# Kernel optimization log

Measured on AMD Instinct MI355X. Metric: run time of the kernel, lower is better.

The kernel has to match this reference:

```python
import jax, jax.numpy as jnp
import numpy as np

NUM_HEADS = 16


def setup_inputs() -> dict:
    key = jax.random.key(0)
    ks = jax.random.split(key, 7)
    dim, hd = 1024, 64
    B, H, W = 64, 14, 14  # B = batch * num_windows, 14x14 window
    x = jax.random.normal(ks[0], (B, H, W, dim), dtype=jnp.float32)
    qkv_w = jax.random.normal(ks[1], (dim, 3 * dim), dtype=jnp.float32) * (dim ** -0.5)
    qkv_b = jnp.zeros((3 * dim,), dtype=jnp.float32)
    proj_w = jax.random.normal(ks[2], (dim, dim), dtype=jnp.float32) * (dim ** -0.5)
    proj_b = jnp.zeros((dim,), dtype=jnp.float32)
    rel_pos_h = jax.random.normal(ks[3], (2 * H - 1, hd), dtype=jnp.float32) * 0.02
    rel_pos_w = jax.random.normal(ks[4], (2 * W - 1, hd), dtype=jnp.float32) * 0.02
    return {"x": x, "qkv_w": qkv_w, "qkv_b": qkv_b, "proj_w": proj_w,
            "proj_b": proj_b, "rel_pos_h": rel_pos_h, "rel_pos_w": rel_pos_w}


def reference(x, qkv_w, qkv_b, proj_w, proj_b, rel_pos_h, rel_pos_w):
    B, H, W, dim = x.shape
    nH = NUM_HEADS
    hd = dim // nH
    scale = hd ** -0.5

    # qkv projection: [B, HW, 3*dim]
    qkv = x.reshape(B, H * W, dim) @ qkv_w + qkv_b
    # -> [3, nH, B, HW, hd] -> [3, nH*B, HW, hd]
    qkv = qkv.reshape(B, H * W, 3, nH, hd).transpose(2, 3, 0, 1, 4)
    qkv = qkv.reshape(3, nH * B, H * W, hd)
    q, k, v = qkv[0], qkv[1], qkv[2]

    # scaled QK^T: [nH*B, HW, HW]
    attn = jnp.einsum('bqc,bkc->bqk', q * scale, k)

    # decomposed relative position bias (q_size == k_size, no interpolation)
    Rh = rel_pos_h[jnp.arange(H)[:, None] - jnp.arange(H)[None, :] + (H - 1)]  # [H,H,hd]
    Rw = rel_pos_w[jnp.arange(W)[:, None] - jnp.arange(W)[None, :] + (W - 1)]  # [W,W,hd]
    r_q = q.reshape(nH * B, H, W, hd)
    rel_h = jnp.einsum('bhwc,hkc->bhwk', r_q, Rh)  # [nH*B,H,W,H]
    rel_w = jnp.einsum('bhwc,wkc->bhwk', r_q, Rw)  # [nH*B,H,W,W]
    attn = (attn.reshape(nH * B, H, W, H, W)
            + rel_h[:, :, :, :, None]
            + rel_w[:, :, :, None, :]).reshape(nH * B, H * W, H * W)

    attn = jax.nn.softmax(attn, axis=-1)
    out = attn @ v  # [nH*B, HW, hd]

    # merge heads: [nH,B,H,W,hd] -> [B,H,W,dim]
    out = out.reshape(nH, B, H, W, hd).transpose(1, 2, 3, 0, 4).reshape(B, H, W, dim)
    return out @ proj_w + proj_b
```

## Files before the change

### kernel.cpp

```cpp
#include <hip/hip_runtime.h>
#include <cstdint>
#include <cstddef>

typedef unsigned short u16;
typedef unsigned int u32;
typedef float f32x4 __attribute__((ext_vector_type(4)));
typedef float f32x2 __attribute__((ext_vector_type(2)));
typedef short short8 __attribute__((ext_vector_type(8)));

#define HW 196
#define DIM 1024
#define HD 64
#define SP 208
#define SPV 224
#define NBH 1024

__device__ __forceinline__ float bf2f(u16 x){
  union { u32 u; float f; } c; c.u = ((u32)x) << 16; return c.f;
}
__device__ __forceinline__ u16 f2bf(float f){
  union { float f; u32 u; } c; c.f = f;
  return (u16)((c.u + 0x7fffu + ((c.u >> 16) & 1u)) >> 16);
}
__device__ __forceinline__ u32 cvtpk_bf16(float lo, float hi){
  u32 r;
  asm("v_cvt_pk_bf16_f32 %0, %1, %2" : "=v"(r) : "v"(lo), "v"(hi));
  return r;
}
#define LGKM_FENCE() do { \
    asm volatile("s_waitcnt lgkmcnt(0)" ::: "memory"); \
    __builtin_amdgcn_sched_barrier(0); \
  } while (0)
#define WAITV4() asm volatile("s_waitcnt vmcnt(4)" ::: "memory")
#define BAR() __builtin_amdgcn_s_barrier()

typedef __attribute__((address_space(3))) void lds_void_t;
typedef __attribute__((address_space(1))) const void glb_void_t;
__device__ __forceinline__ void gload_lds16(const void* g, void* l){
  __builtin_amdgcn_global_load_lds((glb_void_t*)g, (lds_void_t*)l, 16, 0, 0);
}

__global__ __launch_bounds__(256) void k_xcvt(const float* __restrict__ x,
                                              u16* __restrict__ xb, int n8){
  int i = blockIdx.x * 256 + threadIdx.x;
  if (i < n8){
    const f32x4* p = (const f32x4*)(x + (size_t)i * 8);
    f32x4 v0 = p[0], v1 = p[1];
    short8 t;
    #pragma unroll
    for (int e = 0; e < 4; ++e){
      t[e]   = (short)f2bf(v0[e]);
      t[4+e] = (short)f2bf(v1[e]);
    }
    *(short8*)(xb + (size_t)i * 8) = t;
  }
}

__global__ __launch_bounds__(256) void k_rprep(const float* __restrict__ rph,
                                               const float* __restrict__ rpw,
                                               u16* __restrict__ rphb,
                                               u16* __restrict__ rpwb){
  int r = threadIdx.x >> 3, cc = (threadIdx.x & 7) * 8;
  #pragma unroll
  for (int t = 0; t < 2; ++t){
    const float* src = t ? rpw : rph;
    u16* dst = t ? rpwb : rphb;
    short8 v;
    #pragma unroll
    for (int e = 0; e < 8; ++e)
      v[e] = (r < 27) ? (short)f2bf(src[(size_t)r * 64 + cc + e]) : (short)0;
    *(short8*)(dst + (size_t)r * 64 + cc) = v;
  }
}

__global__ __launch_bounds__(256) void k_wT(const float* __restrict__ w,
                                            u16* __restrict__ wT, int K, int N){
  __shared__ float t[32][33];
  int n0 = blockIdx.x * 32, k0 = blockIdx.y * 32;
  int c = threadIdx.x & 31, rr = threadIdx.x >> 5;
  #pragma unroll
  for (int i = 0; i < 4; ++i){
    int r = rr + i*8;
    t[r][c] = w[(size_t)(k0 + r) * N + n0 + c];
  }
  __syncthreads();
  #pragma unroll
  for (int i = 0; i < 4; ++i){
    int r = rr + i*8;
    wT[(size_t)(n0 + r) * K + k0 + c] = f2bf(t[c][r]);
  }
}

template<int MODE, bool SW>
__global__ __launch_bounds__(512, 2) void k_g256(const u16* __restrict__ Ab,
    const u16* __restrict__ Bt, const float* __restrict__ bias,
    u16* __restrict__ qg, u16* __restrict__ kg, u16* __restrict__ vTg,
    float* __restrict__ outf, int K, int N, int ntm, int ntn, int cyoff)
{
  extern __shared__ __align__(16) u16 smem[];
  const int tid = threadIdx.x;
  const int lane = tid & 63, wv = tid >> 6;
  const int wr = wv >> 2, wc = wv & 3;
  const int l16 = lane & 15, lk = lane >> 4;

  const int nwg = ntm * ntn;
  int bid = blockIdx.x;
  int q8 = nwg >> 3, r8 = nwg & 7;
  int xcd = bid & 7, loc = bid >> 3;
  int wgid = (xcd < r8 ? xcd*(q8+1) : r8*(q8+1) + (xcd - r8)*q8) + loc;
  int gsz = 8 * ntn;
  int g = wgid / gsz, rem = wgid - g * gsz;
  int gm = ntm - g * 8; if (gm > 8) gm = 8;
  int ry = g * 8 + rem % gm;
  int cy = rem / gm;
  const size_t m0 = (size_t)ry * 256;
  const size_t n0 = (size_t)(cyoff + cy) * 256;
  const int nk = K >> 6;

  auto off = [&](int d, int ab, int ks){ return ((d*2 + ab)*2 + ks) * 8192; };

  auto stageH = [&](int d, int ab, int ks, int tile){
    const u16* src = ab ? Bt : Ab;
    size_t rb = ab ? n0 : m0;
    int c = (lane & 3) ^ ((lane >> 3) & 3);
    #pragma unroll
    for (int i = 0; i < 2; ++i){
      int rh = 32*wv + 16*i + (lane >> 2);
      gload_lds16(src + (rb + rh) * (size_t)K + tile*64 + ks*32 + c*8,
                  smem + off(d, ab, ks) + (32*wv + 16*i) * 32);
    }
  };
  auto ldA = [&](short8* a, int d, int ks, int h){
    #pragma unroll
    for (int m2 = 0; m2 < 4; ++m2){
      int r = wr*128 + h*64 + m2*16 + l16;
      a[m2] = *(const short8*)(smem + off(d,0,ks) + r*32 + ((lk ^ ((r>>1)&3)) << 3));
    }
  };
  auto ldB = [&](short8* b, int d, int ks){
    #pragma unroll
    for (int ni = 0; ni < 4; ++ni){
      int r = wc*64 + ni*16 + l16;
      b[ni] = *(const short8*)(smem + off(d,1,ks) + r*32 + ((lk ^ ((r>>1)&3)) << 3));
    }
  };

  f32x4 acc[8][4] = {};
  auto mm = [&](int h, short8* a, short8* b){
    __builtin_amdgcn_s_setprio(1);
    #pragma unroll
    for (int m2 = 0; m2 < 4; ++m2)
      #pragma unroll
      for (int ni = 0; ni < 4; ++ni){
        if constexpr (SW)
          acc[h*4+m2][ni] = __builtin_amdgcn_mfma_f32_16x16x32_bf16(b[ni], a[m2], acc[h*4+m2][ni], 0, 0, 0);
        else
          acc[h*4+m2][ni] = __builtin_amdgcn_mfma_f32_16x16x32_bf16(a[m2], b[ni], acc[h*4+m2][ni], 0, 0, 0);
      }
    __builtin_amdgcn_s_setprio(0);
  };

  stageH(0, 0, 0, 0); stageH(0, 1, 0, 0); stageH(0, 0, 1, 0); stageH(0, 1, 1, 0);
  WAITV4(); BAR();

  #pragma unroll 1
  for (int kt = 0; kt < nk; ++kt){
    const int d = kt & 1, dn = d ^ 1;
    const int tn = (kt + 1 < nk) ? kt + 1 : nk - 1;
    short8 a[4], b0[4], b1[4];
    ldA(a, d, 0, 0); ldB(b0, d, 0);
    stageH(dn, 0, 0, tn);
    BAR(); LGKM_FENCE();
    mm(0, a, b0);
    BAR();
    ldA(a, d, 0, 1);
    stageH(dn, 1, 0, tn);
    WAITV4();
    BAR(); LGKM_FENCE();
    mm(1, a, b0);
    BAR();
    ldA(a, d, 1, 0); ldB(b1, d, 1);
    stageH(dn, 0, 1, tn);
    BAR(); LGKM_FENCE();
    mm(0, a, b1);
    BAR();
    ldA(a, d, 1, 1);
    stageH(dn, 1, 1, tn);
    WAITV4();
    BAR(); LGKM_FENCE();
    mm(1, a, b1);
    BAR();
  }

  const int rowb = (int)m0 + wr*128;
  const int colb = (int)n0 + wc*64;
  if constexpr (MODE == 1){
    #pragma unroll
    for (int mi = 0; mi < 8; ++mi){
      int r = rowb + mi*16 + l16;
      float* orow = outf + (size_t)r * N;
      #pragma unroll
      for (int ni = 0; ni < 4; ++ni){
        int c0 = colb + ni*16 + lk*4;
        f32x4 bz = *(const f32x4*)(bias + c0);
        f32x4 v = acc[mi][ni] + bz;
        *(f32x4*)(orow + c0) = v;
      }
    }
  } else if constexpr (SW){
    const int t3 = colb >> 10;
    u16* dst0 = (t3 == 0) ? qg : kg;
    #pragma unroll
    for (int mi = 0; mi < 8; ++mi){
      int r = rowb + mi*16 + l16;
      int b = r / 196, n = r - b * 196;
      #pragma unroll
      for (int ni = 0; ni < 4; ++ni){
        int rr2 = ((colb & 1023) + ni*16);
        int hh = rr2 >> 6, ccb = (rr2 & 63) + lk*4;
        const float* bz = bias + colb + ni*16 + lk*4;
        u32 w0 = cvtpk_bf16(acc[mi][ni][0] + bz[0], acc[mi][ni][1] + bz[1]);
        u32 w1 = cvtpk_bf16(acc[mi][ni][2] + bz[2], acc[mi][ni][3] + bz[3]);
        u32* dst = (u32*)(dst0 + ((size_t)(hh*64 + b) * SP + n) * HD + ccb);
        dst[0] = w0; dst[1] = w1;
      }
    }
  } else {
    #pragma unroll
    for (int mi = 0; mi < 8; ++mi){
      int r4 = rowb + mi*16 + lk*4;
      int b = r4 / 196, n4 = r4 - b * 196;
      #pragma unroll
      for (int ni = 0; ni < 4; ++ni){
        int rr2 = ((colb & 1023) + ni*16);
        int hh = rr2 >> 6, cc = (rr2 & 63) + l16;
        float bz = bias[colb + ni*16 + l16];
        u32 w0 = cvtpk_bf16(acc[mi][ni][0] + bz, acc[mi][ni][1] + bz);
        u32 w1 = cvtpk_bf16(acc[mi][ni][2] + bz, acc[mi][ni][3] + bz);
        u32* dst = (u32*)(vTg + ((size_t)(hh*64 + b) * HD + cc) * SPV + n4);
        dst[0] = w0; dst[1] = w1;
      }
    }
  }
}

__global__ __launch_bounds__(256) void k_attn(
    const u16* __restrict__ qg, const u16* __restrict__ kg, const u16* __restrict__ vTg,
    const u16* __restrict__ rphb, const u16* __restrict__ rpwb,
    u16* __restrict__ ao)
{
  __shared__ __align__(16) char smem[4 * 7168];
  const int tid = threadIdx.x, lane = tid & 63, wvi = tid >> 6;
  const int l16 = lane & 15, lk = lane >> 4;
  char*  wbase = smem + wvi * 7168;
  float* relT  = (float*)wbase;
  float* relg  = (float*)(wbase + 4160);
  char*  pbase = wbase;

  int b = blockIdx.x;
  int sb = (b & 7) * 416 + (b >> 3);
  int j  = sb * 4 + wvi;
  int bh = j / 13;
  int mt = j - bh * 13;
  const int hh = bh >> 6, bb = bh & 63;
  const u16* qb = qg  + (size_t)bh * SP * HD;
  const u16* kb = kg  + (size_t)bh * SP * HD;
  const u16* vb = vTg + (size_t)bh * HD * SPV;

  const short8 a0 = *(const short8*)(qb + (size_t)(mt*16 + l16) * HD + lk*8);
  const short8 a1 = *(const short8*)(qb + (size_t)(mt*16 + l16) * HD + 32 + lk*8);

  {
    f32x4 z = {0.f,0.f,0.f,0.f};
    f32x4 racc[2][2] = {{z,z},{z,z}};
    #pragma unroll
    for (int dt = 0; dt < 2; ++dt){
      short8 h0 = *(const short8*)(rphb + (size_t)(dt*16 + l16) * 64 + lk*8);
      short8 h1 = *(const short8*)(rphb + (size_t)(dt*16 + l16) * 64 + 32 + lk*8);
      short8 w0 = *(const short8*)(rpwb + (size_t)(dt*16 + l16) * 64 + lk*8);
      short8 w1 = *(const short8*)(rpwb + (size_t)(dt*16 + l16) * 64 + 32 + lk*8);
      racc[0][dt] = __builtin_amdgcn_mfma_f32_16x16x32_bf16(h0, a0, racc[0][dt], 0, 0, 0);
      racc[0][dt] = __builtin_amdgcn_mfma_f32_16x16x32_bf16(h1, a1, racc[0][dt], 0, 0, 0);
      racc[1][dt] = __builtin_amdgcn_mfma_f32_16x16x32_bf16(w0, a0, racc[1][dt], 0, 0, 0);
      racc[1][dt] = __builtin_amdgcn_mfma_f32_16x16x32_bf16(w1, a1, racc[1][dt], 0, 0, 0);
    }
    #pragma unroll
    for (int t = 0; t < 2; ++t)
      #pragma unroll
      for (int dt = 0; dt < 2; ++dt)
        #pragma unroll
        for (int i = 0; i < 4; ++i)
          relT[l16*65 + t*32 + dt*16 + lk*4 + i] = racc[t][dt][i];
  }
  LGKM_FENCE();

  {
    int qr = mt*16 + l16;
    int qh = qr / 14, qw = qr - 14*qh;
    #pragma unroll
    for (int c = 0; c < 7; ++c){
      int jj = lk*7 + c;
      int ah = l16*65 + (qh + 13 - jj);
      int aw = l16*65 + 32 + (qw + 27 - jj);
      float v = relT[(jj < 14) ? ah : aw];
      relg[l16*29 + jj] = v;
    }
  }
  LGKM_FENCE();

  f32x4 z = {0.f, 0.f, 0.f, 0.f};
  f32x4 sacc[13];
  #pragma unroll
  for (int nt = 0; nt < 13; ++nt) sacc[nt] = z;
  #pragma unroll
  for (int nt = 0; nt < 13; ++nt){
    int row = nt*16 + l16;
    short8 b0 = *(const short8*)(kb + (size_t)row * HD + lk*8);
    short8 b1 = *(const short8*)(kb + (size_t)row * HD + 32 + lk*8);
    sacc[nt] = __builtin_amdgcn_mfma_f32_16x16x32_bf16(a0, b0, sacc[nt], 0, 0, 0);
    sacc[nt] = __builtin_amdgcn_mfma_f32_16x16x32_bf16(a1, b1, sacc[nt], 0, 0, 0);
  }

  #pragma unroll
  for (int nt = 0; nt < 13; ++nt){
    int key = nt*16 + l16;
    int kh = key / 14, kw = key - 14*kh;
    bool kok = key < HW;
    #pragma unroll
    for (int i = 0; i < 4; ++i){
      int rl = lk*4 + i;
      float s = sacc[nt][i] * 0.125f + relg[rl*29 + kh] + relg[rl*29 + 14 + kw];
      sacc[nt][i] = kok ? s : -1e30f;
    }
  }

  #pragma unroll
  for (int i = 0; i < 4; ++i){
    float m = -1e30f;
    #pragma unroll
    for (int nt = 0; nt < 13; ++nt) m = fmaxf(m, sacc[nt][i]);
    #pragma unroll
    for (int d = 1; d < 16; d <<= 1) m = fmaxf(m, __shfl_xor(m, d, 64));
    float sum = 0.f;
    #pragma unroll
    for (int nt = 0; nt < 13; ++nt){
      float p = __expf(sacc[nt][i] - m);
      sacc[nt][i] = p; sum += p;
    }
    #pragma unroll
    for (int d = 1; d < 16; d <<= 1) sum += __shfl_xor(sum, d, 64);
    float inv = 1.f / sum;
    #pragma unroll
    for (int nt = 0; nt < 13; ++nt) sacc[nt][i] *= inv;
  }

  #pragma unroll
  for (int nt = 0; nt < 14; ++nt){
    #pragma unroll
    for (int i = 0; i < 4; ++i){
      int prow = lk*4 + i;
      int key = nt*16 + l16;
      float pv = (nt < 13) ? sacc[nt][i] : 0.f;
      if (key >= HW || mt*16 + prow >= HW) pv = 0.f;
      int c2 = key * 2;
      if (nt < 12) c2 ^= (prow & 7) << 4;
      *(u16*)(pbase + prow*448 + c2) = f2bf(pv);
    }
  }
  LGKM_FENCE();

  f32x4 oacc[4];
  #pragma unroll
  for (int n = 0; n < 4; ++n) oacc[n] = z;
  #pragma unroll
  for (int kt = 0; kt < 7; ++kt){
    int c2 = kt*64 + lk*16;
    if (kt < 6) c2 ^= (l16 & 7) << 4;
    short8 pa = *(const short8*)(pbase + l16*448 + c2);
    #pragma unroll
    for (int dt = 0; dt < 4; ++dt){
      short8 bv = *(const short8*)(vb + (size_t)(dt*16 + l16) * SPV + kt*32 + lk*8);
      oacc[dt] = __builtin_amdgcn_mfma_f32_16x16x32_bf16(bv, pa, oacc[dt], 0, 0, 0);
    }
  }
  int qrow = mt*16 + l16;
  if (qrow < HW){
    u16* orow = ao + ((size_t)bb * HW + qrow) * DIM + hh * HD;
    #pragma unroll
    for (int dt = 0; dt < 4; ++dt){
      u32 lo = cvtpk_bf16(oacc[dt][0], oacc[dt][1]);
      u32 hi = cvtpk_bf16(oacc[dt][2], oacc[dt][3]);
      u32* dst = (u32*)(orow + dt*16 + lk*4);
      dst[0] = lo; dst[1] = hi;
    }
  }
}

extern "C" void kernel_launch(void* const* d_in, const int* in_sizes, int n_in,
                              void* d_out, int out_size, void* d_ws, size_t ws_size,
                              hipStream_t stream)
{
  const float* x      = (const float*)d_in[0];
  const float* qkv_w  = (const float*)d_in[1];
  const float* qkv_b  = (const float*)d_in[2];
  const float* proj_w = (const float*)d_in[3];
  const float* proj_b = (const float*)d_in[4];
  const float* rph    = (const float*)d_in[5];
  const float* rpw    = (const float*)d_in[6];
  float* out = (float*)d_out;
  char* ws = (char*)d_ws;

  size_t off = 0;
  auto alloc = [&](size_t b){ size_t r = off; off += (b + 255) & ~(size_t)255; return r; };
  u16* wqkvT = (u16*)(ws + alloc((size_t)3072*1024*2));
  u16* wprojT= (u16*)(ws + alloc((size_t)1024*1024*2));
  u16* qg    = (u16*)(ws + alloc((size_t)NBH*SP*HD*2));
  u16* kg    = (u16*)(ws + alloc((size_t)NBH*SP*HD*2));
  u16* vTg   = (u16*)(ws + alloc((size_t)NBH*HD*SPV*2));
  u16* rphb  = (u16*)(ws + alloc((size_t)32*64*2));
  u16* rpwb  = (u16*)(ws + alloc((size_t)32*64*2));
  u16* xb    = (u16*)(ws + alloc((size_t)12544*1024*2));
  u16* ao    = xb;

  hipFuncSetAttribute((const void*)k_g256<0,true>,  hipFuncAttributeMaxDynamicSharedMemorySize, 131072);
  hipFuncSetAttribute((const void*)k_g256<0,false>, hipFuncAttributeMaxDynamicSharedMemorySize, 131072);
  hipFuncSetAttribute((const void*)k_g256<1,true>,  hipFuncAttributeMaxDynamicSharedMemorySize, 131072);

  hipMemsetAsync(vTg, 0, (size_t)NBH*HD*SPV*2, stream);

  k_xcvt<<<(12544*1024/8 + 255)/256, 256, 0, stream>>>(x, xb, 12544*1024/8);
  k_wT<<<dim3(96, 32), 256, 0, stream>>>(qkv_w, wqkvT, 1024, 3072);
  k_wT<<<dim3(32, 32), 256, 0, stream>>>(proj_w, wprojT, 1024, 1024);
  k_rprep<<<1, 256, 0, stream>>>(rph, rpw, rphb, rpwb);

  k_g256<0,true><<<49*8, 512, 131072, stream>>>(xb, wqkvT, qkv_b, qg, kg, nullptr, nullptr,
                                                1024, 3072, 49, 8, 0);
  k_g256<0,false><<<49*4, 512, 131072, stream>>>(xb, wqkvT, qkv_b, nullptr, nullptr, vTg, nullptr,
                                                 1024, 3072, 49, 4, 8);
  k_attn<<<3328, 256, 0, stream>>>(qg, kg, vTg, rphb, rpwb, ao);
  k_g256<1,true><<<49*4, 512, 131072, stream>>>(ao, wprojT, proj_b, nullptr, nullptr, nullptr, out,
                                                1024, 1024, 49, 4, 0);
}
```

Baseline: 260.2 us.

## Transpose score MFMA, fold scale into K, defer softmax normalization

The score MFMA operands are swapped so each lane holds one query row across keys. Row max and sum then need only two cross-lane shuffles instead of four per element group, and the relative-position bias is read straight from the per-row table to seed the accumulators. The 1/8 scale is folded into K during the QKV epilogue. Softmax normalization moves to the output store, and P is written as packed bf16 pairs without swizzling. This removes the relg gather pass, the per-element scaling, and many shuffles and scalar LDS stores, at the cost of possible LDS bank conflicts on the unswizzled P layout and a slightly larger shared-memory footprint.

```diff
diff --git a/kernel.cpp b/kernel.cpp
--- a/kernel.cpp
+++ b/kernel.cpp
@@ -5,8 +5,8 @@
 typedef unsigned short u16;
 typedef unsigned int u32;
 typedef float f32x4 __attribute__((ext_vector_type(4)));
-typedef float f32x2 __attribute__((ext_vector_type(2)));
 typedef short short8 __attribute__((ext_vector_type(8)));
+typedef u32 u32x2 __attribute__((ext_vector_type(2)));
 
 #define HW 196
 #define DIM 1024
@@ -30,6 +30,10 @@
 #define LGKM_FENCE() do { \
     asm volatile("s_waitcnt lgkmcnt(0)" ::: "memory"); \
     __builtin_amdgcn_sched_barrier(0); \
+  } while (0)
+#define DS_FENCE() do { \
+    asm volatile("s_waitcnt lgkmcnt(0)" ::: "memory"); \
+    __builtin_amdgcn_sched_barrier(0x7F); \
   } while (0)
 #define WAITV4() asm volatile("s_waitcnt vmcnt(4)" ::: "memory")
 #define BAR() __builtin_amdgcn_s_barrier()
@@ -210,6 +214,7 @@
   } else if constexpr (SW){
     const int t3 = colb >> 10;
     u16* dst0 = (t3 == 0) ? qg : kg;
+    const float sc = (t3 == 0) ? 1.0f : 0.125f;
     #pragma unroll
     for (int mi = 0; mi < 8; ++mi){
       int r = rowb + mi*16 + l16;
@@ -219,8 +224,8 @@
         int rr2 = ((colb & 1023) + ni*16);
         int hh = rr2 >> 6, ccb = (rr2 & 63) + lk*4;
         const float* bz = bias + colb + ni*16 + lk*4;
-        u32 w0 = cvtpk_bf16(acc[mi][ni][0] + bz[0], acc[mi][ni][1] + bz[1]);
-        u32 w1 = cvtpk_bf16(acc[mi][ni][2] + bz[2], acc[mi][ni][3] + bz[3]);
+        u32 w0 = cvtpk_bf16((acc[mi][ni][0] + bz[0])*sc, (acc[mi][ni][1] + bz[1])*sc);
+        u32 w1 = cvtpk_bf16((acc[mi][ni][2] + bz[2])*sc, (acc[mi][ni][3] + bz[3])*sc);
         u32* dst = (u32*)(dst0 + ((size_t)(hh*64 + b) * SP + n) * HD + ccb);
         dst[0] = w0; dst[1] = w1;
       }
@@ -249,13 +254,12 @@
     const u16* __restrict__ rphb, const u16* __restrict__ rpwb,
     u16* __restrict__ ao)
 {
-  __shared__ __align__(16) char smem[4 * 7168];
+  __shared__ __align__(16) char smem[4 * 7424];
   const int tid = threadIdx.x, lane = tid & 63, wvi = tid >> 6;
   const int l16 = lane & 15, lk = lane >> 4;
-  char*  wbase = smem + wvi * 7168;
+  char*  wbase = smem + wvi * 7424;
   float* relT  = (float*)wbase;
-  float* relg  = (float*)(wbase + 4160);
-  char*  pbase = wbase;
+  u32*   Pp    = (u32*)wbase;
 
   int b = blockIdx.x;
   int sb = (b & 7) * 416 + (b >> 3);
@@ -288,95 +292,88 @@
     for (int t = 0; t < 2; ++t)
       #pragma unroll
       for (int dt = 0; dt < 2; ++dt)
-        #pragma unroll
-        for (int i = 0; i < 4; ++i)
-          relT[l16*65 + t*32 + dt*16 + lk*4 + i] = racc[t][dt][i];
-  }
-  LGKM_FENCE();
-
-  {
-    int qr = mt*16 + l16;
-    int qh = qr / 14, qw = qr - 14*qh;
-    #pragma unroll
-    for (int c = 0; c < 7; ++c){
-      int jj = lk*7 + c;
-      int ah = l16*65 + (qh + 13 - jj);
-      int aw = l16*65 + 32 + (qw + 27 - jj);
-      float v = relT[(jj < 14) ? ah : aw];
-      relg[l16*29 + jj] = v;
-    }
-  }
-  LGKM_FENCE();
-
-  f32x4 z = {0.f, 0.f, 0.f, 0.f};
+        *(f32x4*)(relT + l16*68 + t*32 + dt*16 + lk*4) = racc[t][dt];
+  }
+  DS_FENCE();
+
+  int qr = mt*16 + l16;
+  int qrc = qr > HW-1 ? HW-1 : qr;
+  int qh = qrc / 14, qw = qrc - 14*qh;
+  const float* rrow = relT + l16*68;
+  const int dh0 = qh + 13, dw0 = 32 + qw + 13;
+  const int lk4 = lk*4;
+
   f32x4 sacc[13];
   #pragma unroll
-  for (int nt = 0; nt < 13; ++nt) sacc[nt] = z;
+  for (int nt = 0; nt < 13; ++nt){
+    #pragma unroll
+    for (int i = 0; i < 4; ++i){
+      int k = nt*16 + lk4 + i;
+      int kh = (k * 4682) >> 16;
+      if (nt == 12 && kh > 13) kh = 13;
+      int kw = k - kh*14;
+      float bias = rrow[dh0 - kh] + rrow[dw0 - kw];
+      sacc[nt][i] = (nt == 12 && lk != 0) ? -1e30f : bias;
+    }
+  }
+
   #pragma unroll
   for (int nt = 0; nt < 13; ++nt){
     int row = nt*16 + l16;
     short8 b0 = *(const short8*)(kb + (size_t)row * HD + lk*8);
     short8 b1 = *(const short8*)(kb + (size_t)row * HD + 32 + lk*8);
-    sacc[nt] = __builtin_amdgcn_mfma_f32_16x16x32_bf16(a0, b0, sacc[nt], 0, 0, 0);
-    sacc[nt] = __builtin_amdgcn_mfma_f32_16x16x32_bf16(a1, b1, sacc[nt], 0, 0, 0);
-  }
-
+    sacc[nt] = __builtin_amdgcn_mfma_f32_16x16x32_bf16(b0, a0, sacc[nt], 0, 0, 0);
+    sacc[nt] = __builtin_amdgcn_mfma_f32_16x16x32_bf16(b1, a1, sacc[nt], 0, 0, 0);
+  }
+
+  float m;
+  {
+    float t0[13];
+    #pragma unroll
+    for (int nt = 0; nt < 13; ++nt)
+      t0[nt] = fmaxf(fmaxf(sacc[nt][0], sacc[nt][1]), fmaxf(sacc[nt][2], sacc[nt][3]));
+    float a01 = fmaxf(t0[0], t0[1]),  a23 = fmaxf(t0[2], t0[3]);
+    float a45 = fmaxf(t0[4], t0[5]),  a67 = fmaxf(t0[6], t0[7]);
+    float a89 = fmaxf(t0[8], t0[9]),  aab = fmaxf(t0[10], t0[11]);
+    m = fmaxf(fmaxf(fmaxf(a01, a23), fmaxf(a45, a67)), fmaxf(fmaxf(a89, aab), t0[12]));
+  }
+  m = fmaxf(m, __shfl_xor(m, 16, 64));
+  m = fmaxf(m, __shfl_xor(m, 32, 64));
+  float sum;
+  {
+    float s4[13];
+    #pragma unroll
+    for (int nt = 0; nt < 13; ++nt){
+      #pragma unroll
+      for (int i = 0; i < 4; ++i)
+        sacc[nt][i] = __expf(sacc[nt][i] - m);
+      s4[nt] = (sacc[nt][0] + sacc[nt][1]) + (sacc[nt][2] + sacc[nt][3]);
+    }
+    float b01 = s4[0]+s4[1], b23 = s4[2]+s4[3], b45 = s4[4]+s4[5];
+    float b67 = s4[6]+s4[7], b89 = s4[8]+s4[9], bab = s4[10]+s4[11];
+    sum = ((b01+b23) + (b45+b67)) + ((b89+bab) + s4[12]);
+  }
+  sum += __shfl_xor(sum, 16, 64);
+  sum += __shfl_xor(sum, 32, 64);
+  float inv = 1.0f / sum;
+
+  DS_FENCE();
+  u32* prow = Pp + l16*116;
   #pragma unroll
   for (int nt = 0; nt < 13; ++nt){
-    int key = nt*16 + l16;
-    int kh = key / 14, kw = key - 14*kh;
-    bool kok = key < HW;
-    #pragma unroll
-    for (int i = 0; i < 4; ++i){
-      int rl = lk*4 + i;
-      float s = sacc[nt][i] * 0.125f + relg[rl*29 + kh] + relg[rl*29 + 14 + kw];
-      sacc[nt][i] = kok ? s : -1e30f;
-    }
-  }
-
-  #pragma unroll
-  for (int i = 0; i < 4; ++i){
-    float m = -1e30f;
-    #pragma unroll
-    for (int nt = 0; nt < 13; ++nt) m = fmaxf(m, sacc[nt][i]);
-    #pragma unroll
-    for (int d = 1; d < 16; d <<= 1) m = fmaxf(m, __shfl_xor(m, d, 64));
-    float sum = 0.f;
-    #pragma unroll
-    for (int nt = 0; nt < 13; ++nt){
-      float p = __expf(sacc[nt][i] - m);
-      sacc[nt][i] = p; sum += p;
-    }
-    #pragma unroll
-    for (int d = 1; d < 16; d <<= 1) sum += __shfl_xor(sum, d, 64);
-    float inv = 1.f / sum;
-    #pragma unroll
-    for (int nt = 0; nt < 13; ++nt) sacc[nt][i] *= inv;
-  }
-
-  #pragma unroll
-  for (int nt = 0; nt < 14; ++nt){
-    #pragma unroll
-    for (int i = 0; i < 4; ++i){
-      int prow = lk*4 + i;
-      int key = nt*16 + l16;
-      float pv = (nt < 13) ? sacc[nt][i] : 0.f;
-      if (key >= HW || mt*16 + prow >= HW) pv = 0.f;
-      int c2 = key * 2;
-      if (nt < 12) c2 ^= (prow & 7) << 4;
-      *(u16*)(pbase + prow*448 + c2) = f2bf(pv);
-    }
-  }
-  LGKM_FENCE();
-
-  f32x4 oacc[4];
-  #pragma unroll
-  for (int n = 0; n < 4; ++n) oacc[n] = z;
+    u32x2 wpk;
+    wpk[0] = cvtpk_bf16(sacc[nt][0], sacc[nt][1]);
+    wpk[1] = cvtpk_bf16(sacc[nt][2], sacc[nt][3]);
+    *(u32x2*)(prow + nt*8 + lk*2) = wpk;
+  }
+  { u32x2 zz = {0u, 0u}; *(u32x2*)(prow + 104 + lk*2) = zz; }
+  DS_FENCE();
+
+  f32x4 z = {0.f,0.f,0.f,0.f};
+  f32x4 oacc[4] = {z,z,z,z};
   #pragma unroll
   for (int kt = 0; kt < 7; ++kt){
-    int c2 = kt*64 + lk*16;
-    if (kt < 6) c2 ^= (l16 & 7) << 4;
-    short8 pa = *(const short8*)(pbase + l16*448 + c2);
+    short8 pa = *(const short8*)(prow + kt*16 + lk4);
     #pragma unroll
     for (int dt = 0; dt < 4; ++dt){
       short8 bv = *(const short8*)(vb + (size_t)(dt*16 + l16) * SPV + kt*32 + lk*8);
@@ -388,9 +385,9 @@
     u16* orow = ao + ((size_t)bb * HW + qrow) * DIM + hh * HD;
     #pragma unroll
     for (int dt = 0; dt < 4; ++dt){
-      u32 lo = cvtpk_bf16(oacc[dt][0], oacc[dt][1]);
-      u32 hi = cvtpk_bf16(oacc[dt][2], oacc[dt][3]);
-      u32* dst = (u32*)(orow + dt*16 + lk*4);
+      u32 lo = cvtpk_bf16(oacc[dt][0]*inv, oacc[dt][1]*inv);
+      u32 hi = cvtpk_bf16(oacc[dt][2]*inv, oacc[dt][3]*inv);
+      u32* dst = (u32*)(orow + dt*16 + lk4);
       dst[0] = lo; dst[1] = hi;
     }
   }
```

Measured after the change: 257.1 us. Within noise of the previous version (-1.2%).
